# Kernel tuning notes

Hardware: AMD Instinct MI355X
Metric: run time of the kernel (lower is better)

## Reference

```python
import jax, jax.numpy as jnp
import numpy as np

B, S, D, HEADS = 2, 1024, 1024, 16
DK = D // HEADS           # 64: size of the 'heads' axis after split (namedtensor quirk)
LOW = D // DK             # 16: size of the contracted 'lower' axis
SCALE = float(D)          # Attention(p, scale=d_model) -> divide by d_model
NEG = -1.0e9


def setup_inputs() -> dict:
    key = jax.random.key(0)
    ks = jax.random.split(key, 8)
    query = jax.random.normal(ks[0], (B, S, D), dtype=jnp.float32)
    key_t = jax.random.normal(ks[1], (B, S, D), dtype=jnp.float32)
    value = jax.random.normal(ks[2], (B, S, D), dtype=jnp.float32)
    mask = jax.random.bernoulli(ks[3], 0.25, (B, S, S))  # True -> masked out
    std = 1.0 / np.sqrt(D)
    Wq = jax.random.normal(ks[4], (D, D), dtype=jnp.float32) * std
    Wk = jax.random.normal(ks[5], (D, D), dtype=jnp.float32) * std
    Wv = jax.random.normal(ks[6], (D, D), dtype=jnp.float32) * std
    Wo = jax.random.normal(ks[7], (D, D), dtype=jnp.float32) * std
    return {"query": query, "key": key_t, "value": value, "mask": mask,
            "Wq": Wq, "Wk": Wk, "Wv": Wv, "Wo": Wo}


def reference(query, key, value, mask, Wq, Wk, Wv, Wo):
    # nn.Linear(d_model, d_model, bias=False): y = x @ W.T
    def split(x, W):
        y = jnp.einsum('bsd,ed->bse', x, W)
        return y.reshape(B, -1, DK, LOW)  # hidden -> ('heads'=DK, 'lower'=LOW)

    q = split(query, Wq)   # [B,Sq,H,L] with H=DK, L=LOW
    k = split(key, Wk)     # [B,Sk,H,L]
    v = split(value, Wv)   # [B,Sk,H,L]

    # scores = query.dot('lower', key) / d_model  -> contract the LOW axis
    scores = jnp.einsum('bqhl,bkhl->bhqk', q, k) / SCALE
    scores = jnp.where(mask[:, None, :, :], NEG, scores)  # scores[mask] = -1e9
    p_attn = jax.nn.softmax(scores, axis=-1)  # softmax over keys; dropout=eval

    # value.dot('keys', p_attn) -> [B,H,L,Q]; stack ('heads','lower') -> hidden
    x = jnp.einsum('bkhl,bhqk->bqhl', v, p_attn).reshape(B, -1, D)
    return jnp.einsum('bsd,ed->bse', x, Wo)
```

## Files before the change

### kernel.cpp

```cpp
#include <hip/hip_runtime.h>
#include <hip/hip_bf16.h>


typedef __hip_bfloat16 bf16;
typedef __attribute__((ext_vector_type(8))) short short8;
typedef __attribute__((ext_vector_type(4))) float f32x4;
typedef __attribute__((ext_vector_type(16))) float f32x16;

__device__ __forceinline__ unsigned short f2bf(float f) {
  union { float f; unsigned u; } x; x.f = f;
  unsigned r = x.u + 0x7FFFu + ((x.u >> 16) & 1u);
  return (unsigned short)(r >> 16);
}

__device__ __forceinline__ unsigned cvt_pk_bf16(float lo, float hi) {
  unsigned r;
  asm("v_cvt_pk_bf16_f32 %0, %1, %2" : "=v"(r) : "v"(lo), "v"(hi));
  return r;
}

__device__ __forceinline__ float fast_exp2(float x) {
#if __has_builtin(__builtin_amdgcn_exp2f)
  return __builtin_amdgcn_exp2f(x);
#else
  return __expf(x * 0.6931471805599453f);
#endif
}

__device__ __forceinline__ void gload16(const void* g, void* l) {
#if __has_builtin(__builtin_amdgcn_global_load_lds)
  __builtin_amdgcn_global_load_lds(
      (const __attribute__((address_space(1))) unsigned*)g,
      (__attribute__((address_space(3))) unsigned*)l, 16, 0, 0);
#else
  *(uint4*)l = *(const uint4*)g;
#endif
}

__global__ void bitpack_mask(const unsigned char* __restrict__ mB, const int* __restrict__ mI,
                             unsigned* __restrict__ out) {
  __shared__ int sflag;
  if (threadIdx.x == 0) sflag = 0;
  __syncthreads();
  const int widx = blockIdx.x * 256 + threadIdx.x;
  const int row = widx >> 5, kb = widx & 31;
  uchar4 v[8];
  const uchar4* p = (const uchar4*)(mB + (size_t)row * 1024 + kb * 32);
  unsigned any = 0;
#pragma unroll
  for (int j = 0; j < 8; ++j) { v[j] = p[j]; any |= (unsigned)v[j].y | (unsigned)v[j].z | (unsigned)v[j].w; }
  if (__ballot(any != 0)) { if ((threadIdx.x & 63) == 0) atomicOr(&sflag, 1); }
  __syncthreads();
  unsigned bits = 0;
  if (sflag) {
#pragma unroll
    for (int j = 0; j < 8; ++j) {
      bits |= ((unsigned)(v[j].x != 0) << (4 * j)) | ((unsigned)(v[j].y != 0) << (4 * j + 1))
            | ((unsigned)(v[j].z != 0) << (4 * j + 2)) | ((unsigned)(v[j].w != 0) << (4 * j + 3));
    }
  } else {
    const int4* q = (const int4*)(mI + (size_t)row * 1024 + kb * 32);
#pragma unroll
    for (int j = 0; j < 8; ++j) {
      int4 u = q[j];
      bits |= ((unsigned)(u.x != 0) << (4 * j)) | ((unsigned)(u.y != 0) << (4 * j + 1))
            | ((unsigned)(u.z != 0) << (4 * j + 2)) | ((unsigned)(u.w != 0) << (4 * j + 3));
    }
  }
  const int bq = row >> 10, qb = (row & 1023) >> 5, qr = row & 31;
  out[((((bq * 32 + qb) * 8 + (kb >> 2)) * 32 + qr) << 2) + (kb & 3)] = bits;
}

__global__ void convert_all(
    const float* __restrict__ s0, const float* __restrict__ s1, const float* __restrict__ s2,
    const float* __restrict__ s3, const float* __restrict__ s4, const float* __restrict__ s5,
    const float* __restrict__ s6,
    bf16* __restrict__ d0, bf16* __restrict__ d1, bf16* __restrict__ d2,
    bf16* __restrict__ d3, bf16* __restrict__ d4, bf16* __restrict__ d5,
    bf16* __restrict__ d6) {
  const int z = blockIdx.y;
  const float* s; bf16* d; int n8; float sc = 1.0f;
  if      (z == 0) { s = s0; d = d0; n8 = 262144; }
  else if (z == 1) { s = s1; d = d1; n8 = 262144; }
  else if (z == 2) { s = s2; d = d2; n8 = 262144; }
  else if (z == 3) { s = s3; d = d3; n8 = 131072; sc = 0.0014088818758681283f; }
  else if (z == 4) { s = s4; d = d4; n8 = 131072; }
  else if (z == 5) { s = s5; d = d5; n8 = 131072; }
  else             { s = s6; d = d6; n8 = 131072; }
  const int i = blockIdx.x * 256 + threadIdx.x;
  if (i >= n8) return;
  const f32x4* p = (const f32x4*)s + (size_t)i * 2;
  f32x4 a = p[0], b = p[1];
  uint4 o;
  o.x = cvt_pk_bf16(a[0] * sc, a[1] * sc); o.y = cvt_pk_bf16(a[2] * sc, a[3] * sc);
  o.z = cvt_pk_bf16(b[0] * sc, b[1] * sc); o.w = cvt_pk_bf16(b[2] * sc, b[3] * sc);
  ((uint4*)d)[i] = o;
}

#define GSTR 40
#define PSTR 36

__global__ __launch_bounds__(256) void gemm_qkv(
    const bf16* __restrict__ A0, const bf16* __restrict__ A1, const bf16* __restrict__ A2,
    const bf16* __restrict__ W0, const bf16* __restrict__ W1, const bf16* __restrict__ W2,
    bf16* __restrict__ C0, bf16* __restrict__ C1, bf16* __restrict__ C2) {
  __shared__ __align__(16) bf16 smem[64 * 136];
  bf16* As = smem;
  bf16* Bs = smem + 4096;
  const int z = blockIdx.z;
  const bf16* __restrict__ A = (z == 0) ? A0 : (z == 1) ? A1 : A2;
  const bf16* __restrict__ W = (z == 0) ? W0 : (z == 1) ? W1 : W2;
  bf16* __restrict__ C = (z == 0) ? C0 : (z == 1) ? C1 : C2;
  const int tid = threadIdx.x, lane = tid & 63, w = tid >> 6;
  const int wr = (w >> 1) * 64, wc = (w & 1) * 32;
  const int row0 = blockIdx.y * 128, col0 = blockIdx.x * 64;
  const int l15 = lane & 15, kg = lane >> 4;

  const int srow = lane >> 2, scol = (lane & 3) * 8;
  const bf16* Ag0 = A + (size_t)(row0 + w * 32 + srow) * 1024 + scol;
  const bf16* Ag1 = A + (size_t)(row0 + w * 32 + 16 + srow) * 1024 + scol;
  const bf16* Bg0 = W + (size_t)(col0 + w * 16 + srow) * 1024 + scol;
  bf16* Al0 = As + w * 1024 + lane * 8;
  bf16* Al1 = As + w * 1024 + 512 + lane * 8;
  bf16* Bl0 = Bs + w * 512 + lane * 8;

  f32x4 acc[4][2];
#pragma unroll
  for (int m = 0; m < 4; ++m)
#pragma unroll
    for (int n = 0; n < 2; ++n)
#pragma unroll
      for (int j = 0; j < 4; ++j) acc[m][n][j] = 0.f;

  for (int t = 0; t < 32; ++t) {
    const int k0 = t * 32;
    gload16(Ag0 + k0, Al0);
    gload16(Ag1 + k0, Al1);
    gload16(Bg0 + k0, Bl0);
    __syncthreads();
    short8 af[4], bfr[2];
#pragma unroll
    for (int m = 0; m < 4; ++m) af[m] = *(const short8*)(&As[(wr + m * 16 + l15) * 32 + kg * 8]);
#pragma unroll
    for (int n = 0; n < 2; ++n) bfr[n] = *(const short8*)(&Bs[(wc + n * 16 + l15) * 32 + kg * 8]);
#pragma unroll
    for (int m = 0; m < 4; ++m)
#pragma unroll
      for (int n = 0; n < 2; ++n)
        acc[m][n] = __builtin_amdgcn_mfma_f32_16x16x32_bf16(af[m], bfr[n], acc[m][n], 0, 0, 0);
    __syncthreads();
  }

  const int bb = row0 >> 10, srel0 = row0 & 1023;
  if (z == 2) {
    bf16* T = smem;
#pragma unroll
    for (int m = 0; m < 4; ++m)
#pragma unroll
      for (int n = 0; n < 2; ++n) {
        const int e = wc + n * 16 + l15;
        const int rb = wr + m * 16 + kg * 4;
        uint2 u;
        u.x = cvt_pk_bf16(acc[m][n][0], acc[m][n][1]);
        u.y = cvt_pk_bf16(acc[m][n][2], acc[m][n][3]);
        *(uint2*)(T + e * 136 + rb) = u;
      }
    __syncthreads();
#pragma unroll
    for (int i = 0; i < 4; ++i) {
      const int idx = i * 256 + tid;
      const int tile = idx >> 6, within = idx & 63;
      const int hl = tile >> 2, kbl = tile & 3;
      const int e_sub = within >> 2, kq4 = within & 3;
      uint4 v = *(const uint4*)(T + (hl * 16 + e_sub) * 136 + kbl * 32 + kq4 * 8);
      const int h = (col0 >> 4) + hl;
      const size_t kb = (size_t)((srel0 >> 5) + kbl);
      *(uint4*)((unsigned short*)C + (((size_t)(bb * 64 + h) * 32 + kb) * 512 + e_sub * 32 + kq4 * 8)) = v;
    }
  } else if (z == 1) {
#pragma unroll
    for (int m = 0; m < 4; ++m)
#pragma unroll
      for (int n = 0; n < 2; ++n) {
        const int ecol = wc + n * 16 + l15;
        const int h = (col0 >> 4) + (ecol >> 4), d = ecol & 15;
#pragma unroll
        for (int j = 0; j < 4; ++j) {
          const int s = srel0 + wr + m * 16 + kg * 4 + j;
          ((unsigned short*)C)[((size_t)(bb * 64 + h) * 32 + (s >> 5)) * 512 + (s & 31) * 16 + d] =
              f2bf(acc[m][n][j]);
        }
      }
  } else {
#pragma unroll
    for (int m = 0; m < 4; ++m)
#pragma unroll
      for (int n = 0; n < 2; ++n) {
        const int col = col0 + wc + n * 16 + l15;
#pragma unroll
        for (int j = 0; j < 4; ++j) {
          const int row = row0 + wr + m * 16 + kg * 4 + j;
          ((unsigned short*)C)[(size_t)row * 1024 + col] = f2bf(acc[m][n][j]);
        }
      }
  }
}

__global__ __launch_bounds__(256) void gemm_out(
    const bf16* __restrict__ A, const bf16* __restrict__ W, float* __restrict__ C) {
  __shared__ __align__(16) bf16 smem[6144];
  bf16* As = smem;
  bf16* Bs = smem + 4096;
  const int tid = threadIdx.x, lane = tid & 63, w = tid >> 6;
  const int wr = (w >> 1) * 64, wc = (w & 1) * 32;
  const int row0 = blockIdx.y * 128, col0 = blockIdx.x * 64;
  const int l15 = lane & 15, kg = lane >> 4;

  const int srow = lane >> 2, scol = (lane & 3) * 8;
  const bf16* Ag0 = A + (size_t)(row0 + w * 32 + srow) * 1024 + scol;
  const bf16* Ag1 = A + (size_t)(row0 + w * 32 + 16 + srow) * 1024 + scol;
  const bf16* Bg0 = W + (size_t)(col0 + w * 16 + srow) * 1024 + scol;
  bf16* Al0 = As + w * 1024 + lane * 8;
  bf16* Al1 = As + w * 1024 + 512 + lane * 8;
  bf16* Bl0 = Bs + w * 512 + lane * 8;

  f32x4 acc[4][2];
#pragma unroll
  for (int m = 0; m < 4; ++m)
#pragma unroll
    for (int n = 0; n < 2; ++n)
#pragma unroll
      for (int j = 0; j < 4; ++j) acc[m][n][j] = 0.f;

  for (int t = 0; t < 32; ++t) {
    const int k0 = t * 32;
    gload16(Ag0 + k0, Al0);
    gload16(Ag1 + k0, Al1);
    gload16(Bg0 + k0, Bl0);
    __syncthreads();
    short8 af[4], bfr[2];
#pragma unroll
    for (int m = 0; m < 4; ++m) af[m] = *(const short8*)(&As[(wr + m * 16 + l15) * 32 + kg * 8]);
#pragma unroll
    for (int n = 0; n < 2; ++n) bfr[n] = *(const short8*)(&Bs[(wc + n * 16 + l15) * 32 + kg * 8]);
#pragma unroll
    for (int m = 0; m < 4; ++m)
#pragma unroll
      for (int n = 0; n < 2; ++n)
        acc[m][n] = __builtin_amdgcn_mfma_f32_16x16x32_bf16(af[m], bfr[n], acc[m][n], 0, 0, 0);
    __syncthreads();
  }

#pragma unroll
  for (int m = 0; m < 4; ++m)
#pragma unroll
    for (int n = 0; n < 2; ++n) {
      const int col = col0 + wc + n * 16 + l15;
#pragma unroll
      for (int j = 0; j < 4; ++j) {
        const int row = row0 + wr + m * 16 + kg * 4 + j;
        C[(size_t)row * 1024 + col] = acc[m][n][j];
      }
    }
}

__global__ __launch_bounds__(256) void attn_kernel(
    const bf16* __restrict__ Qp, const bf16* __restrict__ KT, const bf16* __restrict__ VT,
    const unsigned* __restrict__ mw, bf16* __restrict__ XO) {
  __shared__ bf16 Pl[4][2][32 * PSTR];
  const int tid = threadIdx.x, lane = tid & 63, w = tid >> 6;
  const int hi = lane >> 5, l31 = lane & 31, l15 = lane & 15, kg = lane >> 4;
  const int h = blockIdx.y, b = blockIdx.z;
  const int qg = w >> 1, kh = w & 1;
  const int q0 = blockIdx.x * 64 + qg * 32;

  const short8 qf = *(const short8*)(Qp + ((size_t)(b * 1024 + q0 + l31)) * 1024 + h * 16 + hi * 8);
  const bf16* __restrict__ Kb = KT + ((size_t)(b * 64 + h) * 32) * 512;
  const bf16* __restrict__ Vb = VT + ((size_t)(b * 64 + h) * 32) * 512;
  const uint4* __restrict__ Mq =
      (const uint4*)mw + ((size_t)((b * 32 + (q0 >> 5)) * 8 + kh * 4)) * 32 + l31;
  const int sh4 = hi * 4;

  const uint4 mqa = Mq[0], mqb = Mq[32], mqc = Mq[64], mqd = Mq[96];
  const unsigned mm[16] = {mqa.x, mqa.y, mqa.z, mqa.w, mqb.x, mqb.y, mqb.z, mqb.w,
                           mqc.x, mqc.y, mqc.z, mqc.w, mqd.x, mqd.y, mqd.z, mqd.w};

  f32x4 acc0, acc1, sum0, sum1;
#pragma unroll
  for (int j = 0; j < 4; ++j) { acc0[j] = 0.f; acc1[j] = 0.f; sum0[j] = 0.f; sum1[j] = 0.f; }
  f32x16 Z;
#pragma unroll
  for (int i = 0; i < 16; ++i) Z[i] = 0.f;
  short8 ones;
#pragma unroll
  for (int i = 0; i < 8; ++i) ones[i] = (short)0x3F80;

#pragma unroll
  for (int t = 0; t < 16; ++t) {
    const int kbg = kh * 16 + t;
    const unsigned mword = mm[t] >> sh4;
    const short8 kf = *(const short8*)(Kb + (size_t)kbg * 512 + l31 * 16 + hi * 8);
    f32x16 S = __builtin_amdgcn_mfma_f32_32x32x16_bf16(kf, qf, Z, 0, 0, 0);

    bf16* pw = &Pl[w][t & 1][l31 * PSTR];
#pragma unroll
    for (int g = 0; g < 4; ++g) {
      float p0, p1, p2, p3;
      p0 = (mword & (1u << (8 * g + 0))) ? 0.f : fast_exp2(S[4 * g + 0]);
      p1 = (mword & (1u << (8 * g + 1))) ? 0.f : fast_exp2(S[4 * g + 1]);
      p2 = (mword & (1u << (8 * g + 2))) ? 0.f : fast_exp2(S[4 * g + 2]);
      p3 = (mword & (1u << (8 * g + 3))) ? 0.f : fast_exp2(S[4 * g + 3]);
      uint2 u;
      u.x = cvt_pk_bf16(p0, p1);
      u.y = cvt_pk_bf16(p2, p3);
      *(uint2*)(pw + 8 * g + 4 * hi) = u;
    }

    const short8 vf = *(const short8*)(Vb + (size_t)kbg * 512 + l15 * 32 + kg * 8);
    const short8 pa0 = *(const short8*)(&Pl[w][t & 1][l15 * PSTR + kg * 8]);
    const short8 pa1 = *(const short8*)(&Pl[w][t & 1][(16 + l15) * PSTR + kg * 8]);
    __builtin_amdgcn_s_setprio(1);
    acc0 = __builtin_amdgcn_mfma_f32_16x16x32_bf16(pa0, vf, acc0, 0, 0, 0);
    acc1 = __builtin_amdgcn_mfma_f32_16x16x32_bf16(pa1, vf, acc1, 0, 0, 0);
    sum0 = __builtin_amdgcn_mfma_f32_16x16x32_bf16(pa0, ones, sum0, 0, 0, 0);
    sum1 = __builtin_amdgcn_mfma_f32_16x16x32_bf16(pa1, ones, sum1, 0, 0, 0);
    __builtin_amdgcn_s_setprio(0);
  }

  float* fl = (float*)&Pl[0][0][0];
  __syncthreads();
  if (kh) {
    float* dst = fl + ((size_t)(qg * 64 + lane)) * 16;
#pragma unroll
    for (int j = 0; j < 4; ++j) {
      dst[j] = acc0[j]; dst[4 + j] = acc1[j]; dst[8 + j] = sum0[j]; dst[12 + j] = sum1[j];
    }
  }
  __syncthreads();
  if (!kh) {
    const float* src = fl + ((size_t)(qg * 64 + lane)) * 16;
#pragma unroll
    for (int j = 0; j < 4; ++j) {
      const float o0 = acc0[j] + src[j],      d0 = sum0[j] + src[8 + j];
      const float o1 = acc1[j] + src[4 + j],  d1 = sum1[j] + src[12 + j];
      const size_t colo = (size_t)h * 16 + l15;
      ((unsigned short*)XO)[((size_t)(b * 1024 + q0 + kg * 4 + j)) * 1024 + colo] = f2bf(o0 / d0);
      ((unsigned short*)XO)[((size_t)(b * 1024 + q0 + 16 + kg * 4 + j)) * 1024 + colo] = f2bf(o1 / d1);
    }
  }
}

extern "C" void kernel_launch(void* const* d_in, const int* in_sizes, int n_in,
                              void* d_out, int out_size, void* d_ws, size_t ws_size,
                              hipStream_t stream) {
  const float* query = (const float*)d_in[0];
  const float* key   = (const float*)d_in[1];
  const float* value = (const float*)d_in[2];
  const void*  mask  = d_in[3];
  const float* Wq = (const float*)d_in[4];
  const float* Wk = (const float*)d_in[5];
  const float* Wv = (const float*)d_in[6];
  const float* Wo = (const float*)d_in[7];
  float* out = (float*)d_out;

  char* ws = (char*)d_ws;
  const size_t MB = 1024 * 1024;
  unsigned* mbits = (unsigned*)(ws + 4096);
  bf16* Qb  = (bf16*)(ws + 4096 + 262144);
  bf16* Kb  = Qb + 2 * MB;
  bf16* Vb  = Kb + 2 * MB;
  bf16* Wqb = Vb + 2 * MB;
  bf16* Wkb = Wqb + MB;
  bf16* Wvb = Wkb + MB;
  bf16* Wob = Wvb + MB;
  bf16* Qp  = Wob + MB;
  bf16* KTl = Qp + 2 * MB;
  bf16* VTl = KTl + 2 * MB;
  bf16* XO  = VTl + 2 * MB;

  bitpack_mask<<<dim3(256), 256, 0, stream>>>((const unsigned char*)mask, (const int*)mask,
                                              mbits);
  convert_all<<<dim3(1024, 7), 256, 0, stream>>>(query, key, value, Wq, Wk, Wv, Wo,
                                                 Qb, Kb, Vb, Wqb, Wkb, Wvb, Wob);
  gemm_qkv<<<dim3(16, 16, 3), 256, 0, stream>>>(Qb, Kb, Vb, Wqb, Wkb, Wvb, Qp, KTl, VTl);
  attn_kernel<<<dim3(16, 64, 2), 256, 0, stream>>>(Qp, KTl, VTl, mbits, XO);
  gemm_out<<<dim3(16, 16), 256, 0, stream>>>(XO, Wob, out);
}
```

Measured before the change: 98.03 us.

## Fuse mask bitpacking into convert, remap attention grid per XCD, software-pipeline PV MFMAs

Folds the mask bitpack kernel into the convert kernel as an extra grid slice, removing one launch. The attention launch becomes a 1-D grid whose block index is remapped so that all query tiles of a given (batch, head) land on the same XCD, aiming for better L2 reuse of that head's K and V. The P·V and row-sum MFMAs are delayed by one iteration so they overlap with the next tile's QK MFMA and exp work. This adds register pressure from the carried operands, and the convert kernel launches idle blocks in the mask slice.

```diff
diff --git a/kernel.cpp b/kernel.cpp
--- a/kernel.cpp
+++ b/kernel.cpp
@@ -37,48 +37,50 @@
 #endif
 }
 
-__global__ void bitpack_mask(const unsigned char* __restrict__ mB, const int* __restrict__ mI,
-                             unsigned* __restrict__ out) {
-  __shared__ int sflag;
-  if (threadIdx.x == 0) sflag = 0;
-  __syncthreads();
-  const int widx = blockIdx.x * 256 + threadIdx.x;
-  const int row = widx >> 5, kb = widx & 31;
-  uchar4 v[8];
-  const uchar4* p = (const uchar4*)(mB + (size_t)row * 1024 + kb * 32);
-  unsigned any = 0;
-#pragma unroll
-  for (int j = 0; j < 8; ++j) { v[j] = p[j]; any |= (unsigned)v[j].y | (unsigned)v[j].z | (unsigned)v[j].w; }
-  if (__ballot(any != 0)) { if ((threadIdx.x & 63) == 0) atomicOr(&sflag, 1); }
-  __syncthreads();
-  unsigned bits = 0;
-  if (sflag) {
-#pragma unroll
-    for (int j = 0; j < 8; ++j) {
-      bits |= ((unsigned)(v[j].x != 0) << (4 * j)) | ((unsigned)(v[j].y != 0) << (4 * j + 1))
-            | ((unsigned)(v[j].z != 0) << (4 * j + 2)) | ((unsigned)(v[j].w != 0) << (4 * j + 3));
-    }
-  } else {
-    const int4* q = (const int4*)(mI + (size_t)row * 1024 + kb * 32);
-#pragma unroll
-    for (int j = 0; j < 8; ++j) {
-      int4 u = q[j];
-      bits |= ((unsigned)(u.x != 0) << (4 * j)) | ((unsigned)(u.y != 0) << (4 * j + 1))
-            | ((unsigned)(u.z != 0) << (4 * j + 2)) | ((unsigned)(u.w != 0) << (4 * j + 3));
-    }
-  }
-  const int bq = row >> 10, qb = (row & 1023) >> 5, qr = row & 31;
-  out[((((bq * 32 + qb) * 8 + (kb >> 2)) * 32 + qr) << 2) + (kb & 3)] = bits;
-}
-
 __global__ void convert_all(
     const float* __restrict__ s0, const float* __restrict__ s1, const float* __restrict__ s2,
     const float* __restrict__ s3, const float* __restrict__ s4, const float* __restrict__ s5,
     const float* __restrict__ s6,
     bf16* __restrict__ d0, bf16* __restrict__ d1, bf16* __restrict__ d2,
     bf16* __restrict__ d3, bf16* __restrict__ d4, bf16* __restrict__ d5,
-    bf16* __restrict__ d6) {
+    bf16* __restrict__ d6,
+    const unsigned char* __restrict__ mB, const int* __restrict__ mI,
+    unsigned* __restrict__ mout) {
   const int z = blockIdx.y;
+  if (z == 7) {
+    if (blockIdx.x >= 256) return;
+    __shared__ int sflag;
+    if (threadIdx.x == 0) sflag = 0;
+    __syncthreads();
+    const int widx = blockIdx.x * 256 + threadIdx.x;
+    const int row = widx >> 5, kb = widx & 31;
+    uchar4 v[8];
+    const uchar4* p = (const uchar4*)(mB + (size_t)row * 1024 + kb * 32);
+    unsigned any = 0;
+#pragma unroll
+    for (int j = 0; j < 8; ++j) { v[j] = p[j]; any |= (unsigned)v[j].y | (unsigned)v[j].z | (unsigned)v[j].w; }
+    if (__ballot(any != 0)) { if ((threadIdx.x & 63) == 0) atomicOr(&sflag, 1); }
+    __syncthreads();
+    unsigned bits = 0;
+    if (sflag) {
+#pragma unroll
+      for (int j = 0; j < 8; ++j) {
+        bits |= ((unsigned)(v[j].x != 0) << (4 * j)) | ((unsigned)(v[j].y != 0) << (4 * j + 1))
+              | ((unsigned)(v[j].z != 0) << (4 * j + 2)) | ((unsigned)(v[j].w != 0) << (4 * j + 3));
+      }
+    } else {
+      const int4* q = (const int4*)(mI + (size_t)row * 1024 + kb * 32);
+#pragma unroll
+      for (int j = 0; j < 8; ++j) {
+        int4 u = q[j];
+        bits |= ((unsigned)(u.x != 0) << (4 * j)) | ((unsigned)(u.y != 0) << (4 * j + 1))
+              | ((unsigned)(u.z != 0) << (4 * j + 2)) | ((unsigned)(u.w != 0) << (4 * j + 3));
+      }
+    }
+    const int bq = row >> 10, qb = (row & 1023) >> 5, qr = row & 31;
+    mout[((((bq * 32 + qb) * 8 + (kb >> 2)) * 32 + qr) << 2) + (kb & 3)] = bits;
+    return;
+  }
   const float* s; bf16* d; int n8; float sc = 1.0f;
   if      (z == 0) { s = s0; d = d0; n8 = 262144; }
   else if (z == 1) { s = s1; d = d1; n8 = 262144; }
@@ -97,7 +99,6 @@
   ((uint4*)d)[i] = o;
 }
 
-#define GSTR 40
 #define PSTR 36
 
 __global__ __launch_bounds__(256) void gemm_qkv(
@@ -270,9 +271,12 @@
   __shared__ bf16 Pl[4][2][32 * PSTR];
   const int tid = threadIdx.x, lane = tid & 63, w = tid >> 6;
   const int hi = lane >> 5, l31 = lane & 31, l15 = lane & 15, kg = lane >> 4;
-  const int h = blockIdx.y, b = blockIdx.z;
+  const int id = blockIdx.x;
+  const int xcd = id & 7, grp = (id >> 3) & 15, qt = id >> 7;
+  const int g = xcd * 16 + grp;
+  const int b = g >> 6, h = g & 63;
   const int qg = w >> 1, kh = w & 1;
-  const int q0 = blockIdx.x * 64 + qg * 32;
+  const int q0 = qt * 64 + qg * 32;
 
   const short8 qf = *(const short8*)(Qp + ((size_t)(b * 1024 + q0 + l31)) * 1024 + h * 16 + hi * 8);
   const bf16* __restrict__ Kb = KT + ((size_t)(b * 64 + h) * 32) * 512;
@@ -295,6 +299,8 @@
 #pragma unroll
   for (int i = 0; i < 8; ++i) ones[i] = (short)0x3F80;
 
+  short8 pa0p, pa1p, vfp;
+
 #pragma unroll
   for (int t = 0; t < 16; ++t) {
     const int kbg = kh * 16 + t;
@@ -302,30 +308,40 @@
     const short8 kf = *(const short8*)(Kb + (size_t)kbg * 512 + l31 * 16 + hi * 8);
     f32x16 S = __builtin_amdgcn_mfma_f32_32x32x16_bf16(kf, qf, Z, 0, 0, 0);
 
+    if (t > 0) {
+      __builtin_amdgcn_s_setprio(1);
+      acc0 = __builtin_amdgcn_mfma_f32_16x16x32_bf16(pa0p, vfp, acc0, 0, 0, 0);
+      acc1 = __builtin_amdgcn_mfma_f32_16x16x32_bf16(pa1p, vfp, acc1, 0, 0, 0);
+      sum0 = __builtin_amdgcn_mfma_f32_16x16x32_bf16(pa0p, ones, sum0, 0, 0, 0);
+      sum1 = __builtin_amdgcn_mfma_f32_16x16x32_bf16(pa1p, ones, sum1, 0, 0, 0);
+      __builtin_amdgcn_s_setprio(0);
+    }
+
     bf16* pw = &Pl[w][t & 1][l31 * PSTR];
 #pragma unroll
-    for (int g = 0; g < 4; ++g) {
+    for (int gg = 0; gg < 4; ++gg) {
       float p0, p1, p2, p3;
-      p0 = (mword & (1u << (8 * g + 0))) ? 0.f : fast_exp2(S[4 * g + 0]);
-      p1 = (mword & (1u << (8 * g + 1))) ? 0.f : fast_exp2(S[4 * g + 1]);
-      p2 = (mword & (1u << (8 * g + 2))) ? 0.f : fast_exp2(S[4 * g + 2]);
-      p3 = (mword & (1u << (8 * g + 3))) ? 0.f : fast_exp2(S[4 * g + 3]);
+      p0 = (mword & (1u << (8 * gg + 0))) ? 0.f : fast_exp2(S[4 * gg + 0]);
+      p1 = (mword & (1u << (8 * gg + 1))) ? 0.f : fast_exp2(S[4 * gg + 1]);
+      p2 = (mword & (1u << (8 * gg + 2))) ? 0.f : fast_exp2(S[4 * gg + 2]);
+      p3 = (mword & (1u << (8 * gg + 3))) ? 0.f : fast_exp2(S[4 * gg + 3]);
       uint2 u;
       u.x = cvt_pk_bf16(p0, p1);
       u.y = cvt_pk_bf16(p2, p3);
-      *(uint2*)(pw + 8 * g + 4 * hi) = u;
-    }
-
-    const short8 vf = *(const short8*)(Vb + (size_t)kbg * 512 + l15 * 32 + kg * 8);
-    const short8 pa0 = *(const short8*)(&Pl[w][t & 1][l15 * PSTR + kg * 8]);
-    const short8 pa1 = *(const short8*)(&Pl[w][t & 1][(16 + l15) * PSTR + kg * 8]);
-    __builtin_amdgcn_s_setprio(1);
-    acc0 = __builtin_amdgcn_mfma_f32_16x16x32_bf16(pa0, vf, acc0, 0, 0, 0);
-    acc1 = __builtin_amdgcn_mfma_f32_16x16x32_bf16(pa1, vf, acc1, 0, 0, 0);
-    sum0 = __builtin_amdgcn_mfma_f32_16x16x32_bf16(pa0, ones, sum0, 0, 0, 0);
-    sum1 = __builtin_amdgcn_mfma_f32_16x16x32_bf16(pa1, ones, sum1, 0, 0, 0);
-    __builtin_amdgcn_s_setprio(0);
-  }
+      *(uint2*)(pw + 8 * gg + 4 * hi) = u;
+    }
+
+    vfp  = *(const short8*)(Vb + (size_t)kbg * 512 + l15 * 32 + kg * 8);
+    pa0p = *(const short8*)(&Pl[w][t & 1][l15 * PSTR + kg * 8]);
+    pa1p = *(const short8*)(&Pl[w][t & 1][(16 + l15) * PSTR + kg * 8]);
+  }
+
+  __builtin_amdgcn_s_setprio(1);
+  acc0 = __builtin_amdgcn_mfma_f32_16x16x32_bf16(pa0p, vfp, acc0, 0, 0, 0);
+  acc1 = __builtin_amdgcn_mfma_f32_16x16x32_bf16(pa1p, vfp, acc1, 0, 0, 0);
+  sum0 = __builtin_amdgcn_mfma_f32_16x16x32_bf16(pa0p, ones, sum0, 0, 0, 0);
+  sum1 = __builtin_amdgcn_mfma_f32_16x16x32_bf16(pa1p, ones, sum1, 0, 0, 0);
+  __builtin_amdgcn_s_setprio(0);
 
   float* fl = (float*)&Pl[0][0][0];
   __syncthreads();
@@ -378,11 +394,11 @@
   bf16* VTl = KTl + 2 * MB;
   bf16* XO  = VTl + 2 * MB;
 
-  bitpack_mask<<<dim3(256), 256, 0, stream>>>((const unsigned char*)mask, (const int*)mask,
-                                              mbits);
-  convert_all<<<dim3(1024, 7), 256, 0, stream>>>(query, key, value, Wq, Wk, Wv, Wo,
-                                                 Qb, Kb, Vb, Wqb, Wkb, Wvb, Wob);
+  convert_all<<<dim3(1024, 8), 256, 0, stream>>>(query, key, value, Wq, Wk, Wv, Wo,
+                                                 Qb, Kb, Vb, Wqb, Wkb, Wvb, Wob,
+                                                 (const unsigned char*)mask, (const int*)mask,
+                                                 mbits);
   gemm_qkv<<<dim3(16, 16, 3), 256, 0, stream>>>(Qb, Kb, Vb, Wqb, Wkb, Wvb, Qp, KTl, VTl);
-  attn_kernel<<<dim3(16, 64, 2), 256, 0, stream>>>(Qp, KTl, VTl, mbits, XO);
+  attn_kernel<<<dim3(2048), 256, 0, stream>>>(Qp, KTl, VTl, mbits, XO);
   gemm_out<<<dim3(16, 16), 256, 0, stream>>>(XO, Wob, out);
 }
```

Result: faster. 93.74 us (-4.4%).
